# Performance work log

Hardware: AMD Instinct MI355X
Metric: run time of the kernel (lower is better)

Reference implementation:

```python
import jax, jax.numpy as jnp
import numpy as np

EMB = 1024
HEADS = 16
WINDOW = 128


def setup_inputs() -> dict:
    key = jax.random.key(0)
    ks = jax.random.split(key, 9)
    B, N = 2, 2048
    s = 0.02
    f32 = jnp.float32
    return {
        "x": jax.random.normal(ks[0], (B, N, EMB), dtype=f32),
        "Wq": jax.random.normal(ks[1], (EMB, EMB), dtype=f32) * s,
        "bq": jnp.zeros((EMB,), dtype=f32),
        "Wk": jax.random.normal(ks[2], (EMB, EMB), dtype=f32) * s,
        "bk": jnp.zeros((EMB,), dtype=f32),
        "Wv": jax.random.normal(ks[3], (EMB, EMB), dtype=f32) * s,
        "bv": jnp.zeros((EMB,), dtype=f32),
        "Wp": jax.random.normal(ks[4], (EMB, EMB), dtype=f32) * s,
        "bp": jnp.zeros((EMB,), dtype=f32),
    }


def reference(x, Wq, bq, Wk, bk, Wv, bv, Wp, bp):
    B, N, E = x.shape
    H = HEADS
    d = E // H

    def proj(W, b):
        # torch nn.Linear: y = x @ W^T + b, then split heads -> [b, h, n, d]
        y = jnp.einsum('bne,fe->bnf', x, W) + b
        return y.reshape(B, N, H, d).transpose(0, 2, 1, 3)

    q = proj(Wq, bq)
    k = proj(Wk, bk)
    v = proj(Wv, bv)

    # full QK^T then mask out-of-window entries (faithful to original)
    energy = jnp.einsum('bhqd,bhkd->bhqk', q, k)  # [B,H,N,N]
    idx = jnp.arange(N)
    out_of_window = jnp.abs(idx[:, None] - idx[None, :]) > WINDOW  # [N,N] bool
    fmin = jnp.finfo(jnp.float32).min
    energy = jnp.where(out_of_window, fmin, energy)

    scaling = jnp.sqrt(jnp.float32(E))  # note: original scales by sqrt(emb_size)
    att = jax.nn.softmax(energy / scaling, axis=-1)

    out = jnp.einsum('bhqk,bhkd->bhqd', att, v)  # [B,H,N,d]
    out = out.transpose(0, 2, 1, 3).reshape(B, N, E)
    return jnp.einsum('bne,fe->bnf', out, Wp) + bp
```

## Files before the change

kernel.cpp:

```cpp
#include <hip/hip_runtime.h>
#include <stdint.h>

#define EMB    1024
#define NHEAD  16
#define HDIM   64
#define NSEQ   2048
#define NBATCH 2
#define WINDOW 128
#define MROWS  (NBATCH * NSEQ)

typedef __attribute__((ext_vector_type(8))) short  bf16x8;
typedef __attribute__((ext_vector_type(4))) float  f32x4;
typedef __attribute__((ext_vector_type(4))) short  short4v;

__device__ __forceinline__ unsigned short f2bf(float f) {
  union { float f; uint32_t u; } c; c.f = f;
  uint32_t u = c.u;
  u += 0x7fffu + ((u >> 16) & 1u);
  return (unsigned short)(u >> 16);
}

#define GLOAD16(g, l) __builtin_amdgcn_global_load_lds( \
    (const __attribute__((address_space(1))) void*)(g), \
    (__attribute__((address_space(3))) void*)(l), 16, 0, 0)

__global__ __launch_bounds__(256) void cvt_all(
    const float* __restrict__ x,
    const float* __restrict__ w0, const float* __restrict__ w1,
    const float* __restrict__ w2, const float* __restrict__ w3,
    unsigned short* __restrict__ xb,
    unsigned short* __restrict__ o0, unsigned short* __restrict__ o1,
    unsigned short* __restrict__ o2, unsigned short* __restrict__ o3) {
  const int i = blockIdx.x * 256 + threadIdx.x;
  const float* src; unsigned short* dst; int off;
  if (i < 1048576) { src = x; dst = xb; off = i; }
  else {
    int j = i - 1048576;
    int sel = j >> 18; off = j & 262143;
    src = sel == 0 ? w0 : sel == 1 ? w1 : sel == 2 ? w2 : w3;
    dst = sel == 0 ? o0 : sel == 1 ? o1 : sel == 2 ? o2 : o3;
  }
  float4 v = ((const float4*)src)[off];
  short4v o;
  o.x = (short)f2bf(v.x);
  o.y = (short)f2bf(v.y);
  o.z = (short)f2bf(v.z);
  o.w = (short)f2bf(v.w);
  ((short4v*)dst)[off] = o;
}

__device__ __forceinline__ void gemm_pipe(const unsigned short* __restrict__ A,
                                          const unsigned short* __restrict__ Bw,
                                          const float* __restrict__ bias,
                                          void* __restrict__ Cv,
                                          int m0, int n0, int mode, float scale) {
  constexpr int K = 1024, BK = 64, NT = K / BK;
  __shared__ char lds[2][32768];
  const int t    = threadIdx.x;
  const int lane = t & 63;
  const int wv   = t >> 6;
  const int lhi  = lane >> 4, llo = lane & 15;
  const int wr   = wv >> 1, wc = wv & 1;

  const unsigned short* gsrc[8];
  int ldsoff[8];
  #pragma unroll
  for (int li = 0; li < 8; ++li) {
    const int isB = li >= 4;
    const int c = (isB ? (li - 4) : li) * 4 + wv;
    const int P = c * 1024 + lane * 16;
    const int L = P ^ (((P >> 7) & 7) << 4);
    const int row = L >> 7, sl = (L >> 4) & 7;
    gsrc[li] = (isB ? Bw + (size_t)(n0 + row) * K : A + (size_t)(m0 + row) * K) + sl * 8;
    ldsoff[li] = isB * 16384 + c * 1024;
  }

  int aoff[2][4], boff[2][4];
  #pragma unroll
  for (int ks = 0; ks < 2; ++ks)
    #pragma unroll
    for (int f = 0; f < 4; ++f) {
      const int ar = wr * 64 + f * 16 + llo;
      aoff[ks][f] = (ar * 128 + ks * 64 + lhi * 16) ^ ((ar & 7) << 4);
      const int bc = wc * 64 + f * 16 + llo;
      boff[ks][f] = 16384 + ((bc * 128 + ks * 64 + lhi * 16) ^ ((bc & 7) << 4));
    }

  const f32x4 zero = {0.f, 0.f, 0.f, 0.f};
  f32x4 acc[4][4];
  #pragma unroll
  for (int i = 0; i < 4; ++i)
    #pragma unroll
    for (int j = 0; j < 4; ++j) acc[i][j] = zero;

  #pragma unroll
  for (int li = 0; li < 8; ++li) GLOAD16(gsrc[li], (char*)lds + ldsoff[li]);
  #pragma unroll
  for (int li = 0; li < 8; ++li) GLOAD16(gsrc[li] + BK, (char*)lds + 32768 + ldsoff[li]);

  for (int t0 = 0; t0 < NT; ++t0) {
    if (t0 + 1 < NT) asm volatile("s_waitcnt vmcnt(8)" ::: "memory");
    else             asm volatile("s_waitcnt vmcnt(0)" ::: "memory");
    asm volatile("s_barrier" ::: "memory");
    __builtin_amdgcn_sched_barrier(0);

    const char* base = (const char*)lds + (t0 & 1) * 32768;
    bf16x8 af[2][4], bg[2][4];
    #pragma unroll
    for (int ks = 0; ks < 2; ++ks)
      #pragma unroll
      for (int f = 0; f < 4; ++f) {
        af[ks][f] = *(const bf16x8*)(base + aoff[ks][f]);
        bg[ks][f] = *(const bf16x8*)(base + boff[ks][f]);
      }
    asm volatile("s_waitcnt lgkmcnt(0)" ::: "memory");
    asm volatile("s_barrier" ::: "memory");
    __builtin_amdgcn_sched_barrier(0);

    if (t0 + 2 < NT) {
      #pragma unroll
      for (int li = 0; li < 8; ++li)
        GLOAD16(gsrc[li] + (t0 + 2) * BK, (char*)lds + (t0 & 1) * 32768 + ldsoff[li]);
    }

    __builtin_amdgcn_s_setprio(1);
    #pragma unroll
    for (int ks = 0; ks < 2; ++ks)
      #pragma unroll
      for (int mf = 0; mf < 4; ++mf)
        #pragma unroll
        for (int nf = 0; nf < 4; ++nf)
          acc[mf][nf] = __builtin_amdgcn_mfma_f32_16x16x32_bf16(af[ks][mf], bg[ks][nf], acc[mf][nf], 0, 0, 0);
    __builtin_amdgcn_s_setprio(0);
  }

  const int wm = wr * 64, wn = wc * 64;
  #pragma unroll
  for (int mf = 0; mf < 4; ++mf) {
    #pragma unroll
    for (int nf = 0; nf < 4; ++nf) {
      const int col = n0 + wn + nf * 16 + llo;
      if (mode == 1) {
        const int row_base = m0 + wm + mf * 16 + lhi * 4;
        const int bb = row_base >> 11, n = row_base & 2047;
        const int hh = col >> 6, dd = col & 63;
        short4v o;
        #pragma unroll
        for (int r = 0; r < 4; ++r) o[r] = (short)f2bf((acc[mf][nf][r] + bias[col]) * scale);
        unsigned short* p = (unsigned short*)Cv +
            ((size_t)((bb * NHEAD + hh) * HDIM + dd)) * NSEQ + n;
        *(short4v*)p = o;
      } else {
        #pragma unroll
        for (int r = 0; r < 4; ++r) {
          const int row = m0 + wm + mf * 16 + lhi * 4 + r;
          const float v = (acc[mf][nf][r] + bias[col]) * scale;
          if (mode == 0) {
            const int bb = row >> 11, n = row & 2047;
            const int hh = col >> 6, dd = col & 63;
            ((unsigned short*)Cv)[((size_t)(bb * NHEAD + hh) * NSEQ + n) * HDIM + dd] = f2bf(v);
          } else {
            ((float*)Cv)[(size_t)row * EMB + col] = v;
          }
        }
      }
    }
  }
}

__global__ __launch_bounds__(256, 2) void gemm_qkv(
    const unsigned short* __restrict__ A,
    const unsigned short* __restrict__ W0, const unsigned short* __restrict__ W1,
    const unsigned short* __restrict__ W2,
    const float* __restrict__ b0, const float* __restrict__ b1, const float* __restrict__ b2,
    unsigned short* __restrict__ O0, unsigned short* __restrict__ O1,
    unsigned short* __restrict__ O2) {
  const int m0 = blockIdx.x * 128, n0 = blockIdx.y * 128;
  const unsigned short* W = (blockIdx.z == 0) ? W0 : (blockIdx.z == 1) ? W1 : W2;
  const float* bb         = (blockIdx.z == 0) ? b0 : (blockIdx.z == 1) ? b1 : b2;
  unsigned short* O       = (blockIdx.z == 0) ? O0 : (blockIdx.z == 1) ? O1 : O2;
  const int mode          = (blockIdx.z == 2) ? 1 : 0;
  const float scale       = (blockIdx.z == 0) ? 0.03125f : 1.0f;
  gemm_pipe(A, W, bb, (void*)O, m0, n0, mode, scale);
}

__global__ __launch_bounds__(256, 2) void gemm_proj(
    const unsigned short* __restrict__ A, const unsigned short* __restrict__ W,
    const float* __restrict__ bias, float* __restrict__ O) {
  gemm_pipe(A, W, bias, (void*)O, blockIdx.x * 128, blockIdx.y * 128, 2, 1.0f);
}

__global__ __launch_bounds__(256, 4) void attn_kernel(
    const unsigned short* __restrict__ Qh, const unsigned short* __restrict__ Kh,
    const unsigned short* __restrict__ Vt, unsigned short* __restrict__ AO) {
  constexpr int NCH = 10;
  __shared__ char kv[2][8192];
  __shared__ unsigned short Pb[4][16 * 32];
  const int t = threadIdx.x;
  const int lane = t & 63, wv = t >> 6;
  const int lhi = lane >> 4, llo = lane & 15;

  const int linear = blockIdx.x + 32 * (blockIdx.y + 16 * blockIdx.z);
  const int xcd = linear & 7, pos = linear >> 3;
  const int plane = xcd * 4 + (pos >> 5);
  const int qblk = pos & 31;
  const int b = plane >> 4, h = plane & 15;
  const int q0b = qblk * 64;
  const int q0 = q0b + wv * 16;

  const size_t pbase = (size_t)plane * NSEQ * HDIM;

  bf16x8 aq0, aq1;
  {
    const unsigned short* qp = Qh + pbase + (size_t)(q0 + llo) * HDIM + 8 * lhi;
    aq0 = *(const bf16x8*)qp;
    aq1 = *(const bf16x8*)(qp + 32);
  }

  const int PK = t * 16;
  const int LK = PK ^ (((PK >> 7) & 7) << 4);
  const int krow_l = LK >> 7;
  const int kslot8 = ((LK >> 4) & 7) * 8;
  const int LV = PK ^ (((PK >> 7) & 3) << 4);
  const int vrow = LV >> 6;
  const int vslot8 = ((LV >> 4) & 3) * 8;

  int koff[2];
  #pragma unroll
  for (int half = 0; half < 2; ++half) {
    const int row = half * 16 + llo;
    koff[half] = (row * 128 + lhi * 16) ^ ((row & 7) << 4);
  }
  int voff[4];
  #pragma unroll
  for (int fd = 0; fd < 4; ++fd) {
    const int row = fd * 16 + llo;
    voff[fd] = 4096 + ((row * 64 + lhi * 16) ^ (((row >> 1) & 3) << 4));
  }

  bf16x8 vones;
  #pragma unroll
  for (int j = 0; j < 8; ++j) vones[j] = (short)0x3F80;

  const f32x4 zero = {0.f, 0.f, 0.f, 0.f};
  f32x4 accv[4];
  f32x4 s_acc = zero;
  #pragma unroll
  for (int i = 0; i < 4; ++i) accv[i] = zero;

  auto stage = [&](int ct, int slot) {
    const int kb = q0b - WINDOW + ct * 32;
    int n = kb + krow_l;
    n = n < 0 ? 0 : (n > NSEQ - 1 ? NSEQ - 1 : n);
    GLOAD16(Kh + pbase + (size_t)n * HDIM + kslot8, (char*)kv[slot] + PK);
    int c = kb + vslot8;
    c = c < 0 ? 0 : (c > NSEQ - 8 ? NSEQ - 8 : c);
    GLOAD16(Vt + pbase + (size_t)vrow * NSEQ + c, (char*)kv[slot] + 4096 + PK);
  };

  stage(0, 0);
  stage(1, 1);

  for (int ct = 0; ct < NCH; ++ct) {
    if (ct + 1 < NCH) asm volatile("s_waitcnt vmcnt(2)" ::: "memory");
    else              asm volatile("s_waitcnt vmcnt(0)" ::: "memory");
    asm volatile("s_barrier" ::: "memory");
    __builtin_amdgcn_sched_barrier(0);

    const char* sb = kv[ct & 1];
    bf16x8 bk[2][2], bv[4];
    #pragma unroll
    for (int half = 0; half < 2; ++half) {
      bk[half][0] = *(const bf16x8*)(sb + koff[half]);
      bk[half][1] = *(const bf16x8*)(sb + (koff[half] ^ 64));
    }
    #pragma unroll
    for (int fd = 0; fd < 4; ++fd) bv[fd] = *(const bf16x8*)(sb + voff[fd]);
    asm volatile("s_waitcnt lgkmcnt(0)" ::: "memory");
    __builtin_amdgcn_sched_barrier(0);
    asm volatile("s_barrier" ::: "memory");
    __builtin_amdgcn_sched_barrier(0);

    if (ct + 2 < NCH) stage(ct + 2, ct & 1);

    const int kb = q0b - WINDOW + ct * 32;
    f32x4 e[2];
    #pragma unroll
    for (int half = 0; half < 2; ++half) {
      f32x4 z = zero;
      z = __builtin_amdgcn_mfma_f32_16x16x32_bf16(aq0, bk[half][0], z, 0, 0, 0);
      z = __builtin_amdgcn_mfma_f32_16x16x32_bf16(aq1, bk[half][1], z, 0, 0, 0);
      e[half] = z;
    }
    f32x4 p0, p1;
    #pragma unroll
    for (int half = 0; half < 2; ++half) {
      const int key = kb + half * 16 + llo;
      #pragma unroll
      for (int r = 0; r < 4; ++r) {
        const int q = q0 + lhi * 4 + r;
        const int dlt = key - q;
        const bool valid = (key >= 0) && (key < NSEQ) && (dlt <= WINDOW) && (dlt >= -WINDOW);
        const float ev = valid ? fminf(e[half][r], 40.f) : -1e30f;
        if (half == 0) p0[r] = __expf(ev); else p1[r] = __expf(ev);
      }
    }

    #pragma unroll
    for (int r = 0; r < 4; ++r) {
      Pb[wv][(lhi * 4 + r) * 32 + llo]      = f2bf(p0[r]);
      Pb[wv][(lhi * 4 + r) * 32 + 16 + llo] = f2bf(p1[r]);
    }
    const bf16x8 pa = *(const bf16x8*)&Pb[wv][llo * 32 + 8 * lhi];

    s_acc = __builtin_amdgcn_mfma_f32_16x16x32_bf16(pa, vones, s_acc, 0, 0, 0);
    #pragma unroll
    for (int fd = 0; fd < 4; ++fd)
      accv[fd] = __builtin_amdgcn_mfma_f32_16x16x32_bf16(pa, bv[fd], accv[fd], 0, 0, 0);
  }

  #pragma unroll
  for (int fd = 0; fd < 4; ++fd) {
    #pragma unroll
    for (int r = 0; r < 4; ++r) {
      const float o = accv[fd][r] / s_acc[r];
      const int q = q0 + lhi * 4 + r;
      AO[((size_t)b * NSEQ + q) * EMB + h * HDIM + fd * 16 + llo] = f2bf(o);
    }
  }
}

extern "C" void kernel_launch(void* const* d_in, const int* in_sizes, int n_in,
                              void* d_out, int out_size, void* d_ws, size_t ws_size,
                              hipStream_t stream) {
  (void)in_sizes; (void)n_in; (void)out_size; (void)ws_size;
  const float* x  = (const float*)d_in[0];
  const float* Wq = (const float*)d_in[1];
  const float* bq = (const float*)d_in[2];
  const float* Wk = (const float*)d_in[3];
  const float* bk = (const float*)d_in[4];
  const float* Wv = (const float*)d_in[5];
  const float* bv = (const float*)d_in[6];
  const float* Wp = (const float*)d_in[7];
  const float* bp = (const float*)d_in[8];
  float* out = (float*)d_out;
  char* ws = (char*)d_ws;
  const size_t MB = 1u << 20;
  unsigned short* xb  = (unsigned short*)(ws + 0 * MB);
  unsigned short* Wqb = (unsigned short*)(ws + 8 * MB);
  unsigned short* Wkb = (unsigned short*)(ws + 10 * MB);
  unsigned short* Wvb = (unsigned short*)(ws + 12 * MB);
  unsigned short* Wpb = (unsigned short*)(ws + 14 * MB);
  unsigned short* Qb  = (unsigned short*)(ws + 16 * MB);
  unsigned short* Kb  = (unsigned short*)(ws + 24 * MB);
  unsigned short* Vtb = (unsigned short*)(ws + 32 * MB);
  unsigned short* AOb = (unsigned short*)(ws + 40 * MB);

  cvt_all<<<dim3(8192), dim3(256), 0, stream>>>(x, Wq, Wk, Wv, Wp,
                                                xb, Wqb, Wkb, Wvb, Wpb);

  gemm_qkv<<<dim3(MROWS / 128, EMB / 128, 3), dim3(256), 0, stream>>>(
      xb, Wqb, Wkb, Wvb, bq, bk, bv, Qb, Kb, Vtb);

  attn_kernel<<<dim3(NSEQ / 64, NHEAD, NBATCH), dim3(256), 0, stream>>>(Qb, Kb, Vtb, AOb);

  gemm_proj<<<dim3(MROWS / 128, EMB / 128), dim3(256), 0, stream>>>(AOb, Wpb, bp, out);
}
```

Baseline: 80.55 us.

## Double attention key chunk to 64 keys with swizzled P buffer and MFMA priority

```diff
diff --git a/kernel.cpp b/kernel.cpp
--- a/kernel.cpp
+++ b/kernel.cpp
@@ -193,9 +193,9 @@
 __global__ __launch_bounds__(256, 4) void attn_kernel(
     const unsigned short* __restrict__ Qh, const unsigned short* __restrict__ Kh,
     const unsigned short* __restrict__ Vt, unsigned short* __restrict__ AO) {
-  constexpr int NCH = 10;
-  __shared__ char kv[2][8192];
-  __shared__ unsigned short Pb[4][16 * 32];
+  constexpr int NCH = 5;
+  __shared__ char kv[2][16384];
+  __shared__ unsigned short Pb[4][1024];
   const int t = threadIdx.x;
   const int lane = t & 63, wv = t >> 6;
   const int lhi = lane >> 4, llo = lane & 15;
@@ -217,26 +217,34 @@
     aq1 = *(const bf16x8*)(qp + 32);
   }
 
-  const int PK = t * 16;
-  const int LK = PK ^ (((PK >> 7) & 7) << 4);
-  const int krow_l = LK >> 7;
-  const int kslot8 = ((LK >> 4) & 7) * 8;
-  const int LV = PK ^ (((PK >> 7) & 3) << 4);
-  const int vrow = LV >> 6;
-  const int vslot8 = ((LV >> 4) & 3) * 8;
-
-  int koff[2];
-  #pragma unroll
-  for (int half = 0; half < 2; ++half) {
+  int srow[4], scol8[4];
+  #pragma unroll
+  for (int li = 0; li < 4; ++li) {
+    const int P = (li & 1) * 4096 + t * 16;
+    const int L = P ^ (((P >> 7) & 7) << 4);
+    srow[li] = L >> 7;
+    scol8[li] = ((L >> 4) & 7) * 8;
+  }
+
+  int koff[4];
+  #pragma unroll
+  for (int half = 0; half < 4; ++half) {
     const int row = half * 16 + llo;
     koff[half] = (row * 128 + lhi * 16) ^ ((row & 7) << 4);
   }
-  int voff[4];
+  int voff[4][2];
   #pragma unroll
   for (int fd = 0; fd < 4; ++fd) {
     const int row = fd * 16 + llo;
-    voff[fd] = 4096 + ((row * 64 + lhi * 16) ^ (((row >> 1) & 3) << 4));
-  }
+    #pragma unroll
+    for (int ks = 0; ks < 2; ++ks)
+      voff[fd][ks] = 8192 + ((row * 128 + ks * 64 + lhi * 16) ^ ((row & 7) << 4));
+  }
+  int paoff[2];
+  #pragma unroll
+  for (int ks = 0; ks < 2; ++ks)
+    paoff[ks] = (llo * 128 + ks * 64 + lhi * 16) ^ ((llo & 7) << 4);
+  char* pb = (char*)&Pb[wv][0];
 
   bf16x8 vones;
   #pragma unroll
@@ -249,74 +257,84 @@
   for (int i = 0; i < 4; ++i) accv[i] = zero;
 
   auto stage = [&](int ct, int slot) {
-    const int kb = q0b - WINDOW + ct * 32;
-    int n = kb + krow_l;
-    n = n < 0 ? 0 : (n > NSEQ - 1 ? NSEQ - 1 : n);
-    GLOAD16(Kh + pbase + (size_t)n * HDIM + kslot8, (char*)kv[slot] + PK);
-    int c = kb + vslot8;
-    c = c < 0 ? 0 : (c > NSEQ - 8 ? NSEQ - 8 : c);
-    GLOAD16(Vt + pbase + (size_t)vrow * NSEQ + c, (char*)kv[slot] + 4096 + PK);
+    const int kb = q0b - WINDOW + ct * 64;
+    #pragma unroll
+    for (int li = 0; li < 2; ++li) {
+      int n = kb + srow[li];
+      n = n < 0 ? 0 : (n > NSEQ - 1 ? NSEQ - 1 : n);
+      GLOAD16(Kh + pbase + (size_t)n * HDIM + scol8[li],
+              (char*)kv[slot] + (li & 1) * 4096 + t * 16);
+    }
+    #pragma unroll
+    for (int li = 2; li < 4; ++li) {
+      int c = kb + scol8[li];
+      c = c < 0 ? 0 : (c > NSEQ - 8 ? NSEQ - 8 : c);
+      GLOAD16(Vt + pbase + (size_t)srow[li] * NSEQ + c,
+              (char*)kv[slot] + 8192 + (li & 1) * 4096 + t * 16);
+    }
   };
 
   stage(0, 0);
   stage(1, 1);
 
   for (int ct = 0; ct < NCH; ++ct) {
-    if (ct + 1 < NCH) asm volatile("s_waitcnt vmcnt(2)" ::: "memory");
+    if (ct + 1 < NCH) asm volatile("s_waitcnt vmcnt(4)" ::: "memory");
     else              asm volatile("s_waitcnt vmcnt(0)" ::: "memory");
     asm volatile("s_barrier" ::: "memory");
     __builtin_amdgcn_sched_barrier(0);
 
     const char* sb = kv[ct & 1];
-    bf16x8 bk[2][2], bv[4];
-    #pragma unroll
-    for (int half = 0; half < 2; ++half) {
-      bk[half][0] = *(const bf16x8*)(sb + koff[half]);
-      bk[half][1] = *(const bf16x8*)(sb + (koff[half] ^ 64));
-    }
-    #pragma unroll
-    for (int fd = 0; fd < 4; ++fd) bv[fd] = *(const bf16x8*)(sb + voff[fd]);
-    asm volatile("s_waitcnt lgkmcnt(0)" ::: "memory");
-    __builtin_amdgcn_sched_barrier(0);
-    asm volatile("s_barrier" ::: "memory");
-    __builtin_amdgcn_sched_barrier(0);
-
-    if (ct + 2 < NCH) stage(ct + 2, ct & 1);
-
-    const int kb = q0b - WINDOW + ct * 32;
-    f32x4 e[2];
-    #pragma unroll
-    for (int half = 0; half < 2; ++half) {
+    const int kb = q0b - WINDOW + ct * 64;
+
+    f32x4 e[4];
+    #pragma unroll
+    for (int half = 0; half < 4; ++half) {
+      bf16x8 k0 = *(const bf16x8*)(sb + koff[half]);
+      bf16x8 k1 = *(const bf16x8*)(sb + (koff[half] ^ 64));
       f32x4 z = zero;
-      z = __builtin_amdgcn_mfma_f32_16x16x32_bf16(aq0, bk[half][0], z, 0, 0, 0);
-      z = __builtin_amdgcn_mfma_f32_16x16x32_bf16(aq1, bk[half][1], z, 0, 0, 0);
+      z = __builtin_amdgcn_mfma_f32_16x16x32_bf16(aq0, k0, z, 0, 0, 0);
+      z = __builtin_amdgcn_mfma_f32_16x16x32_bf16(aq1, k1, z, 0, 0, 0);
       e[half] = z;
     }
-    f32x4 p0, p1;
-    #pragma unroll
-    for (int half = 0; half < 2; ++half) {
+
+    #pragma unroll
+    for (int half = 0; half < 4; ++half) {
       const int key = kb + half * 16 + llo;
       #pragma unroll
       for (int r = 0; r < 4; ++r) {
         const int q = q0 + lhi * 4 + r;
         const int dlt = key - q;
         const bool valid = (key >= 0) && (key < NSEQ) && (dlt <= WINDOW) && (dlt >= -WINDOW);
-        const float ev = valid ? fminf(e[half][r], 40.f) : -1e30f;
-        if (half == 0) p0[r] = __expf(ev); else p1[r] = __expf(ev);
+        const float p = __expf(valid ? fminf(e[half][r], 40.f) : -1e30f);
+        const int row = lhi * 4 + r, col = half * 16 + llo;
+        *(unsigned short*)(pb + ((row * 128 + col * 2) ^ ((row & 7) << 4))) = f2bf(p);
       }
     }
-
-    #pragma unroll
-    for (int r = 0; r < 4; ++r) {
-      Pb[wv][(lhi * 4 + r) * 32 + llo]      = f2bf(p0[r]);
-      Pb[wv][(lhi * 4 + r) * 32 + 16 + llo] = f2bf(p1[r]);
-    }
-    const bf16x8 pa = *(const bf16x8*)&Pb[wv][llo * 32 + 8 * lhi];
-
-    s_acc = __builtin_amdgcn_mfma_f32_16x16x32_bf16(pa, vones, s_acc, 0, 0, 0);
-    #pragma unroll
-    for (int fd = 0; fd < 4; ++fd)
-      accv[fd] = __builtin_amdgcn_mfma_f32_16x16x32_bf16(pa, bv[fd], accv[fd], 0, 0, 0);
+    const bf16x8 pa0 = *(const bf16x8*)(pb + paoff[0]);
+    const bf16x8 pa1 = *(const bf16x8*)(pb + paoff[1]);
+
+    bf16x8 bv[4][2];
+    #pragma unroll
+    for (int fd = 0; fd < 4; ++fd) {
+      bv[fd][0] = *(const bf16x8*)(sb + voff[fd][0]);
+      bv[fd][1] = *(const bf16x8*)(sb + voff[fd][1]);
+    }
+    asm volatile("s_waitcnt lgkmcnt(0)" ::: "memory");
+    __builtin_amdgcn_sched_barrier(0);
+    asm volatile("s_barrier" ::: "memory");
+    __builtin_amdgcn_sched_barrier(0);
+
+    if (ct + 2 < NCH) stage(ct + 2, ct & 1);
+
+    __builtin_amdgcn_s_setprio(1);
+    s_acc = __builtin_amdgcn_mfma_f32_16x16x32_bf16(pa0, vones, s_acc, 0, 0, 0);
+    s_acc = __builtin_amdgcn_mfma_f32_16x16x32_bf16(pa1, vones, s_acc, 0, 0, 0);
+    #pragma unroll
+    for (int fd = 0; fd < 4; ++fd) {
+      accv[fd] = __builtin_amdgcn_mfma_f32_16x16x32_bf16(pa0, bv[fd][0], accv[fd], 0, 0, 0);
+      accv[fd] = __builtin_amdgcn_mfma_f32_16x16x32_bf16(pa1, bv[fd][1], accv[fd], 0, 0, 0);
+    }
+    __builtin_amdgcn_s_setprio(0);
   }
 
   #pragma unroll
```

New measurement: 78.94 us, median of 3. 1.02x faster.
